# Optimization experiments

Hardware: AMD Instinct MI355X
Metric: run time of the kernel (lower is better)

## Reference

```python
import math
import jax, jax.numpy as jnp
import numpy as np

N_NODES = 50000
N_EDGES = 800000
FEAT = 64          # m * p == p * n == 64
P = 8              # product_size
M = FEAT // P      # 8


def setup_inputs() -> dict:
    key = jax.random.key(0)
    k1, k2, k3, k4 = jax.random.split(key, 4)
    src_feat = jax.random.normal(k1, (N_NODES, FEAT), dtype=jnp.float32)
    dst_feat = jax.random.normal(k2, (N_NODES, FEAT), dtype=jnp.float32)
    edge_src = jax.random.randint(k3, (N_EDGES,), 0, N_NODES, dtype=jnp.int32)
    edge_dst = jax.random.randint(k4, (N_EDGES,), 0, N_NODES, dtype=jnp.int32)
    return {"src_feat": src_feat, "dst_feat": dst_feat,
            "edge_src": edge_src, "edge_dst": edge_dst}


def reference(src_feat, dst_feat, edge_src, edge_dst):
    # src.view(..., -1, P) ; dst.view(..., P, -1)
    src = src_feat.reshape(N_NODES, M, P)          # [N, m, p]
    dst = dst_feat.reshape(N_NODES, P, M)          # [N, p, n]
    # per-edge SDDMM-style batched matmul: gather endpoints, matmul
    e_src = src[edge_src]                          # [E, m, p]
    e_dst = dst[edge_dst]                          # [E, p, n]
    ft_e = jnp.einsum('eij,ejk->eik', e_src, e_dst)  # [E, m, n]
    # sum-aggregate edge features onto destination nodes
    agg = jax.ops.segment_sum(ft_e, edge_dst, num_segments=N_NODES)  # [N, m, n]
    result = agg / math.sqrt(P)
    # squeeze: flatten last two dims
    return result.reshape(N_NODES, M * M)
```

## Files before the change

### kernel.cpp

```cpp
#include <hip/hip_runtime.h>
#include <hip/hip_bf16.h>

#define N_NODES 50000
#define N_EDGES 800000
#define FEAT 64
#define CAP 64
#define RANGE 32
#define NBINS 1563
#define K1B 160
#define EPB (N_EDGES / K1B)
#define SUB 32

static __device__ __forceinline__ unsigned short f2bu(float f) {
    __hip_bfloat16 h = __float2bfloat16(f);
    return __builtin_bit_cast(unsigned short, h);
}

__global__ __launch_bounds__(256) void conv_kernel(
    const float* __restrict__ src_feat,
    unsigned short* __restrict__ src16)
{
    int base = (blockIdx.x * 256 + threadIdx.x) * 8;
    if (base >= N_NODES * FEAT) return;
    float4 a = *(const float4*)(src_feat + base);
    float4 b = *(const float4*)(src_feat + base + 4);
    uint4 o;
    o.x = (unsigned)f2bu(a.x) | ((unsigned)f2bu(a.y) << 16);
    o.y = (unsigned)f2bu(a.z) | ((unsigned)f2bu(a.w) << 16);
    o.z = (unsigned)f2bu(b.x) | ((unsigned)f2bu(b.y) << 16);
    o.w = (unsigned)f2bu(b.z) | ((unsigned)f2bu(b.w) << 16);
    *(uint4*)(src16 + base) = o;
}

__global__ __launch_bounds__(256) void bin_kernel(
    const int* __restrict__ edge_src,
    const int* __restrict__ edge_dst,
    int* __restrict__ counts,
    int* __restrict__ ent)
{
    __shared__ int h[NBINS];
    int tid = threadIdx.x;
    int b = blockIdx.x;
    int e0 = b * EPB;
    int e1 = e0 + EPB;

    for (int r = tid; r < NBINS; r += 256) h[r] = 0;
    __syncthreads();

    for (int e = e0 + tid * 4; e < e1; e += 1024) {
        int4 d4 = *(const int4*)(edge_dst + e);
        atomicAdd(&h[d4.x >> 5], 1);
        atomicAdd(&h[d4.y >> 5], 1);
        atomicAdd(&h[d4.z >> 5], 1);
        atomicAdd(&h[d4.w >> 5], 1);
    }
    __syncthreads();

    for (int r = tid; r < NBINS; r += 256) {
        int c = h[r];
        counts[r * K1B + b] = (c > SUB) ? SUB : c;
        h[r] = 0;
    }
    __syncthreads();

    for (int e = e0 + tid * 4; e < e1; e += 1024) {
        int4 s4 = *(const int4*)(edge_src + e);
        int4 d4 = *(const int4*)(edge_dst + e);
        int r0 = d4.x >> 5, r1 = d4.y >> 5, r2 = d4.z >> 5, r3 = d4.w >> 5;
        int p0 = atomicAdd(&h[r0], 1);
        int p1 = atomicAdd(&h[r1], 1);
        int p2 = atomicAdd(&h[r2], 1);
        int p3 = atomicAdd(&h[r3], 1);
        if (p0 < SUB) ent[(r0 * K1B + b) * SUB + p0] = ((d4.x & 31) << 16) | s4.x;
        if (p1 < SUB) ent[(r1 * K1B + b) * SUB + p1] = ((d4.y & 31) << 16) | s4.y;
        if (p2 < SUB) ent[(r2 * K1B + b) * SUB + p2] = ((d4.z & 31) << 16) | s4.z;
        if (p3 < SUB) ent[(r3 * K1B + b) * SUB + p3] = ((d4.w & 31) << 16) | s4.w;
    }
}

__global__ __launch_bounds__(512, 8) void sort_gather_mm_kernel(
    const unsigned short* __restrict__ src16,
    const float* __restrict__ dst_feat,
    const int* __restrict__ counts,
    const int* __restrict__ ent,
    float* __restrict__ out)
{
    __shared__ __align__(16) unsigned short bucket[RANGE * CAP];
    __shared__ int cnt_s[K1B];
    __shared__ int c[RANGE];

    int r = blockIdx.x;
    int tid = threadIdx.x;
    if (tid < RANGE) c[tid] = 0;
    if (tid < K1B) cnt_s[tid] = counts[r * K1B + tid];
    __syncthreads();

    const int* er = ent + (size_t)r * K1B * SUB;
    for (int g = tid; g < K1B * SUB; g += 512) {
        int bb = g >> 5;
        int s  = g & 31;
        if (s < cnt_s[bb]) {
            int p = er[g];
            int dl = p >> 16;
            int pos = atomicAdd(&c[dl], 1);
            if (pos < CAP) bucket[dl * CAP + pos] = (unsigned short)(p & 0xFFFF);
        }
    }
    __syncthreads();

    int wave = tid >> 6;
    int lane = tid & 63;
    int i = lane >> 3;
    int j = lane & 7;

    #pragma unroll
    for (int m = 0; m < 4; ++m) {
        int nl = wave * 4 + m;
        int n = r * RANGE + nl;
        if (n >= N_NODES) break;
        int deg = c[nl];
        if (deg > CAP) deg = CAP;
        const uint4* bk = (const uint4*)(bucket + nl * CAP);

        float B = dst_feat[n * FEAT + lane];

        float acc = 0.0f;
        int t = 0;
        for (; t + 8 <= deg; t += 8) {
            uint4 w = bk[t >> 3];
            int i0 = w.x & 0xFFFF, i1 = w.x >> 16;
            int i2 = w.y & 0xFFFF, i3 = w.y >> 16;
            int i4 = w.z & 0xFFFF, i5 = w.z >> 16;
            int i6 = w.w & 0xFFFF, i7 = w.w >> 16;
            unsigned short u0 = src16[i0 * FEAT + lane];
            unsigned short u1 = src16[i1 * FEAT + lane];
            unsigned short u2 = src16[i2 * FEAT + lane];
            unsigned short u3 = src16[i3 * FEAT + lane];
            unsigned short u4 = src16[i4 * FEAT + lane];
            unsigned short u5 = src16[i5 * FEAT + lane];
            unsigned short u6 = src16[i6 * FEAT + lane];
            unsigned short u7 = src16[i7 * FEAT + lane];
            acc += __uint_as_float((unsigned)u0 << 16);
            acc += __uint_as_float((unsigned)u1 << 16);
            acc += __uint_as_float((unsigned)u2 << 16);
            acc += __uint_as_float((unsigned)u3 << 16);
            acc += __uint_as_float((unsigned)u4 << 16);
            acc += __uint_as_float((unsigned)u5 << 16);
            acc += __uint_as_float((unsigned)u6 << 16);
            acc += __uint_as_float((unsigned)u7 << 16);
        }
        for (; t < deg; ++t) {
            unsigned short u = src16[(int)bucket[nl * CAP + t] * FEAT + lane];
            acc += __uint_as_float((unsigned)u << 16);
        }

        float res = 0.0f;
        #pragma unroll
        for (int p = 0; p < 8; ++p) {
            float s_ip = __shfl(acc, i * 8 + p, 64);
            float b_pj = __shfl(B, p * 8 + j, 64);
            res += s_ip * b_pj;
        }
        out[n * FEAT + lane] = res * 0.35355339059327373f;
    }
}

extern "C" void kernel_launch(void* const* d_in, const int* in_sizes, int n_in,
                              void* d_out, int out_size, void* d_ws, size_t ws_size,
                              hipStream_t stream) {
    const float* src_feat = (const float*)d_in[0];
    const float* dst_feat = (const float*)d_in[1];
    const int* edge_src = (const int*)d_in[2];
    const int* edge_dst = (const int*)d_in[3];
    float* out = (float*)d_out;

    char* w = (char*)d_ws;
    int* counts = (int*)w;                        w += (size_t)NBINS * K1B * 4;
    int* ent = (int*)w;                           w += (size_t)NBINS * K1B * SUB * 4;
    unsigned short* src16 = (unsigned short*)w;


    int blocksConv = (N_NODES * FEAT / 8 + 255) / 256;
    conv_kernel<<<blocksConv, 256, 0, stream>>>(src_feat, src16);

    bin_kernel<<<K1B, 256, 0, stream>>>(edge_src, edge_dst, counts, ent);

    sort_gather_mm_kernel<<<NBINS, 512, 0, stream>>>(
        src16, dst_feat, counts, ent, out);
}
```

Baseline: 123.7 us.

## Replace per-node bucket sort with flat edge list and LDS atomic aggregation

The final kernel no longer sorts each bin's edges into per-node buckets. It compacts the valid edges into one shared list using ballot and popcount. All eight waves then process edges from that list, gathering source rows and accumulating them into a shared fp32 per-node sum with LDS atomicAdd. This spreads the gather work evenly across waves instead of making each wave depend on its own nodes' degrees, and it removes the per-node capacity limit. In exchange it adds LDS float atomics per element and makes the summation order nondeterministic.

```diff
diff --git a/kernel.cpp b/kernel.cpp
--- a/kernel.cpp
+++ b/kernel.cpp
@@ -4,12 +4,12 @@
 #define N_NODES 50000
 #define N_EDGES 800000
 #define FEAT 64
-#define CAP 64
 #define RANGE 32
 #define NBINS 1563
 #define K1B 160
 #define EPB (N_EDGES / K1B)
 #define SUB 32
+#define ECAP 1024
 
 static __device__ __forceinline__ unsigned short f2bu(float f) {
     __hip_bfloat16 h = __float2bfloat16(f);
@@ -78,87 +78,87 @@
     }
 }
 
-__global__ __launch_bounds__(512, 8) void sort_gather_mm_kernel(
+__global__ __launch_bounds__(512, 8) void gather_mm_kernel(
     const unsigned short* __restrict__ src16,
     const float* __restrict__ dst_feat,
     const int* __restrict__ counts,
     const int* __restrict__ ent,
     float* __restrict__ out)
 {
-    __shared__ __align__(16) unsigned short bucket[RANGE * CAP];
+    __shared__ float agg[RANGE * FEAT];
+    __shared__ int elist[ECAP];
     __shared__ int cnt_s[K1B];
-    __shared__ int c[RANGE];
+    __shared__ int nent;
 
     int r = blockIdx.x;
     int tid = threadIdx.x;
-    if (tid < RANGE) c[tid] = 0;
+    int wave = tid >> 6;
+    int lane = tid & 63;
+
+    *(float4*)(agg + tid * 4) = make_float4(0.f, 0.f, 0.f, 0.f);
     if (tid < K1B) cnt_s[tid] = counts[r * K1B + tid];
+    if (tid == 0) nent = 0;
+
+    float Bv[4];
+    #pragma unroll
+    for (int m = 0; m < 4; ++m) {
+        int n = r * RANGE + wave * 4 + m;
+        Bv[m] = (n < N_NODES) ? dst_feat[n * FEAT + lane] : 0.f;
+    }
     __syncthreads();
 
     const int* er = ent + (size_t)r * K1B * SUB;
     for (int g = tid; g < K1B * SUB; g += 512) {
         int bb = g >> 5;
         int s  = g & 31;
-        if (s < cnt_s[bb]) {
-            int p = er[g];
-            int dl = p >> 16;
-            int pos = atomicAdd(&c[dl], 1);
-            if (pos < CAP) bucket[dl * CAP + pos] = (unsigned short)(p & 0xFFFF);
-        }
+        bool valid = (s < cnt_s[bb]);
+        int p = valid ? er[g] : 0;
+        unsigned long long mask = __ballot(valid);
+        int rank = __popcll(mask & ((1ULL << lane) - 1ULL));
+        int cnt  = __popcll(mask);
+        int base;
+        if (lane == 0) base = atomicAdd(&nent, cnt);
+        base = __shfl(base, 0, 64);
+        int pos = base + rank;
+        if (valid && pos < ECAP) elist[pos] = p;
     }
     __syncthreads();
 
-    int wave = tid >> 6;
-    int lane = tid & 63;
+    int ne = nent;
+    if (ne > ECAP) ne = ECAP;
+
+    for (int t = wave * 8; t < ne; t += 64) {
+        int pe[8];
+        float v[8];
+        #pragma unroll
+        for (int u = 0; u < 8; ++u)
+            pe[u] = (t + u < ne) ? elist[t + u] : -1;
+        #pragma unroll
+        for (int u = 0; u < 8; ++u)
+            if (pe[u] >= 0) {
+                unsigned short w = src16[(pe[u] & 0xFFFF) * FEAT + lane];
+                v[u] = __uint_as_float((unsigned)w << 16);
+            }
+        #pragma unroll
+        for (int u = 0; u < 8; ++u)
+            if (pe[u] >= 0)
+                atomicAdd(&agg[(pe[u] >> 16) * FEAT + lane], v[u]);
+    }
+    __syncthreads();
+
     int i = lane >> 3;
     int j = lane & 7;
-
     #pragma unroll
     for (int m = 0; m < 4; ++m) {
         int nl = wave * 4 + m;
         int n = r * RANGE + nl;
         if (n >= N_NODES) break;
-        int deg = c[nl];
-        if (deg > CAP) deg = CAP;
-        const uint4* bk = (const uint4*)(bucket + nl * CAP);
-
-        float B = dst_feat[n * FEAT + lane];
-
-        float acc = 0.0f;
-        int t = 0;
-        for (; t + 8 <= deg; t += 8) {
-            uint4 w = bk[t >> 3];
-            int i0 = w.x & 0xFFFF, i1 = w.x >> 16;
-            int i2 = w.y & 0xFFFF, i3 = w.y >> 16;
-            int i4 = w.z & 0xFFFF, i5 = w.z >> 16;
-            int i6 = w.w & 0xFFFF, i7 = w.w >> 16;
-            unsigned short u0 = src16[i0 * FEAT + lane];
-            unsigned short u1 = src16[i1 * FEAT + lane];
-            unsigned short u2 = src16[i2 * FEAT + lane];
-            unsigned short u3 = src16[i3 * FEAT + lane];
-            unsigned short u4 = src16[i4 * FEAT + lane];
-            unsigned short u5 = src16[i5 * FEAT + lane];
-            unsigned short u6 = src16[i6 * FEAT + lane];
-            unsigned short u7 = src16[i7 * FEAT + lane];
-            acc += __uint_as_float((unsigned)u0 << 16);
-            acc += __uint_as_float((unsigned)u1 << 16);
-            acc += __uint_as_float((unsigned)u2 << 16);
-            acc += __uint_as_float((unsigned)u3 << 16);
-            acc += __uint_as_float((unsigned)u4 << 16);
-            acc += __uint_as_float((unsigned)u5 << 16);
-            acc += __uint_as_float((unsigned)u6 << 16);
-            acc += __uint_as_float((unsigned)u7 << 16);
-        }
-        for (; t < deg; ++t) {
-            unsigned short u = src16[(int)bucket[nl * CAP + t] * FEAT + lane];
-            acc += __uint_as_float((unsigned)u << 16);
-        }
-
+        float S = agg[nl * FEAT + lane];
         float res = 0.0f;
         #pragma unroll
         for (int p = 0; p < 8; ++p) {
-            float s_ip = __shfl(acc, i * 8 + p, 64);
-            float b_pj = __shfl(B, p * 8 + j, 64);
+            float s_ip = __shfl(S, i * 8 + p, 64);
+            float b_pj = __shfl(Bv[m], p * 8 + j, 64);
             res += s_ip * b_pj;
         }
         out[n * FEAT + lane] = res * 0.35355339059327373f;
@@ -179,12 +179,11 @@
     int* ent = (int*)w;                           w += (size_t)NBINS * K1B * SUB * 4;
     unsigned short* src16 = (unsigned short*)w;
 
-
     int blocksConv = (N_NODES * FEAT / 8 + 255) / 256;
     conv_kernel<<<blocksConv, 256, 0, stream>>>(src_feat, src16);
 
     bin_kernel<<<K1B, 256, 0, stream>>>(edge_src, edge_dst, counts, ent);
 
-    sort_gather_mm_kernel<<<NBINS, 512, 0, stream>>>(
+    gather_mm_kernel<<<NBINS, 512, 0, stream>>>(
         src16, dst_feat, counts, ent, out);
 }
```

New measurement: 416.0 us. 3.36x slower.
